# Kernel tuning notes

Hardware: AMD Instinct MI355X
Metric: run time of the kernel (lower is better)

## Reference

```python
import jax, jax.numpy as jnp
import numpy as np
from jax import lax

DISP = 4   # max displacement for correlation -> 81 channels
KSZ = 3    # deform/gate conv kernel size


def conv2d(x, w, b=None):
    out = lax.conv_general_dilated(x, w, (1, 1), 'SAME',
                                   dimension_numbers=('NCHW', 'OIHW', 'NCHW'))
    if b is not None:
        out = out + b[None, :, None, None]
    return out


def correlation(x1, x2, d=DISP):
    # FlowNet-style cost volume, kernel_size=1: per-displacement channel-mean dot product.
    B, C, H, W = x1.shape
    x2p = jnp.pad(x2, ((0, 0), (0, 0), (d, d), (d, d)))
    outs = []
    for dy in range(2 * d + 1):
        for dx in range(2 * d + 1):
            shifted = lax.dynamic_slice(x2p, (0, 0, dy, dx), (B, C, H, W))
            outs.append(jnp.sum(x1 * shifted, axis=1) / C)
    return jnp.stack(outs, axis=1)  # [B, (2d+1)^2, H, W]


def bilinear_sample(img, y, x):
    # img: [B,C,H,W]; y,x: [B,H,W] float sample coords; zero padding outside.
    B, C, H, W = img.shape
    y0 = jnp.floor(y); x0 = jnp.floor(x)
    y1 = y0 + 1.0;     x1 = x0 + 1.0
    wy1 = y - y0; wx1 = x - x0
    wy0 = 1.0 - wy1; wx0 = 1.0 - wx1
    flat = img.reshape(B, C, H * W)

    def gather(yi, xi):
        valid = (yi >= 0) & (yi <= H - 1) & (xi >= 0) & (xi <= W - 1)
        yc = jnp.clip(yi, 0, H - 1).astype(jnp.int32)
        xc = jnp.clip(xi, 0, W - 1).astype(jnp.int32)
        idx = (yc * W + xc).reshape(B, 1, H * W)
        g = jnp.take_along_axis(flat, idx, axis=2).reshape(B, C, H, W)
        return g * valid.astype(img.dtype)[:, None]

    return (gather(y0, x0) * (wy0 * wx0)[:, None]
          + gather(y0, x1) * (wy0 * wx1)[:, None]
          + gather(y1, x0) * (wy1 * wx0)[:, None]
          + gather(y1, x1) * (wy1 * wx1)[:, None])


def deform_conv(img, offset, w, k=KSZ):
    # offset: [B, 2*k*k, H, W] with (dy, dx) pairs per kernel tap (row-major).
    B, C, H, W = img.shape
    pad = (k - 1) // 2
    ys = jnp.arange(H, dtype=img.dtype)[None, :, None]
    xs = jnp.arange(W, dtype=img.dtype)[None, None, :]
    out = jnp.zeros((B, w.shape[0], H, W), dtype=img.dtype)
    for kk in range(k * k):
        ky, kx = kk // k, kk % k
        y = ys + (ky - pad) + offset[:, 2 * kk]
        x = xs + (kx - pad) + offset[:, 2 * kk + 1]
        s = bilinear_sample(img, y, x)
        out = out + jnp.einsum('oc,bchw->bohw', w[:, :, ky, kx], s)
    return out


def linear_scale(x, std_multiplier=3.0):
    pos = x > 0
    cnt = jnp.sum(pos).astype(x.dtype)
    mean = jnp.sum(jnp.where(pos, x, 0.0)) / jnp.maximum(cnt, 1.0)
    var = jnp.sum(jnp.where(pos, (x - mean) ** 2, 0.0)) / jnp.maximum(cnt - 1.0, 1.0)
    ub = mean + std_multiplier * jnp.sqrt(var)
    ub = jnp.where(cnt >= 2.0, ub, 1.0)  # matches torch nan / empty-positive fallback
    return jnp.clip(x, 0.0, lax.stop_gradient(ub)) / ub


def setup_inputs() -> dict:
    key = jax.random.key(0)
    ks = jax.random.split(key, 10)
    B, C, H, W = 8, 256, 64, 64
    f = jnp.float32
    inp = {
        'inputs':   jax.random.normal(ks[0], (B, C, H, W), f),
        'in_state': jax.random.normal(ks[1], (B, C, H, W), f),
        'w_reset':  jax.random.normal(ks[2], (C, 2 * C, 3, 3), f) * 0.02,
        'b_reset':  jnp.zeros((C,), f),
        'w_update': jax.random.normal(ks[3], (C, 2 * C, 3, 3), f) * 0.02,
        'b_update': jnp.zeros((C,), f),
        'w_out':    jax.random.normal(ks[4], (C, 2 * C, 3, 3), f) * 0.02,
        'b_out':    jnp.zeros((C,), f),
        'w_offset': jax.random.normal(ks[5], (18, 81, 1, 1), f) * 0.01,
        'w_align':  jax.random.normal(ks[6], (C, C, 3, 3), f) * 0.01,
    }
    return inp


def reference(inputs, in_state, w_reset, b_reset, w_update, b_update,
              w_out, b_out, w_offset, w_align):
    # align_features: correlation -> 1x1 offset conv -> deformable conv
    corr = correlation(inputs, in_state)
    offset = conv2d(corr, w_offset)
    aligned = deform_conv(in_state, offset, w_align)
    # ConvGRU gates with linear-scaled relu gates
    stacked = jnp.concatenate([inputs, aligned], axis=1)
    update = linear_scale(jax.nn.relu(conv2d(stacked, w_update, b_update)))
    reset = linear_scale(jax.nn.relu(conv2d(stacked, w_reset, b_reset)))
    out_in = jax.nn.relu(conv2d(jnp.concatenate([inputs, in_state * reset], axis=1), w_out, b_out))
    new_state = in_state * (1.0 - update) + out_in * update
    return (new_state, new_state)  # (out_feat, new_state)
```

## Files before the change

kernel.cpp:

```cpp
#include <hip/hip_runtime.h>
#include <stdint.h>
#include <math.h>

typedef unsigned short u16;
typedef short bf16x8 __attribute__((ext_vector_type(8)));
typedef float f32x4 __attribute__((ext_vector_type(4)));

#define MFMA16x16x32(a,b,c) __builtin_amdgcn_mfma_f32_16x16x32_bf16((a),(b),(c),0,0,0)

typedef __attribute__((address_space(3))) void as3_void;
typedef const __attribute__((address_space(1))) void as1_void;

__device__ __forceinline__ void g2l16(const void* g, void* l){
#if __has_builtin(__builtin_amdgcn_global_load_lds)
  __builtin_amdgcn_global_load_lds((as1_void*)g, (as3_void*)l, 16, 0, 0);
#else
  *(int4*)l = *(const int4*)g;
#endif
}

__device__ __forceinline__ u16 f2bf(float f){
  uint32_t u = __builtin_bit_cast(uint32_t, f);
  u += 0x7fffu + ((u >> 16) & 1u);
  return (u16)(u >> 16);
}
__device__ __forceinline__ float bf2f(u16 h){
  uint32_t u = ((uint32_t)h) << 16;
  return __builtin_bit_cast(float, u);
}
__device__ __forceinline__ void unpack8(int4 v, float* o){
  uint32_t w0=(uint32_t)v.x, w1=(uint32_t)v.y, w2=(uint32_t)v.z, w3=(uint32_t)v.w;
  o[0]=__builtin_bit_cast(float, w0<<16); o[1]=__builtin_bit_cast(float, w0&0xffff0000u);
  o[2]=__builtin_bit_cast(float, w1<<16); o[3]=__builtin_bit_cast(float, w1&0xffff0000u);
  o[4]=__builtin_bit_cast(float, w2<<16); o[5]=__builtin_bit_cast(float, w2&0xffff0000u);
  o[6]=__builtin_bit_cast(float, w3<<16); o[7]=__builtin_bit_cast(float, w3&0xffff0000u);
}
__device__ __forceinline__ int iclampi(int v,int lo,int hi){ return v<lo?lo:(v>hi?hi:v); }

__global__ void k_repack(const float* __restrict__ w_reset, const float* __restrict__ b_reset,
                         const float* __restrict__ w_update, const float* __restrict__ b_update,
                         const float* __restrict__ w_out, const float* __restrict__ w_offset,
                         const float* __restrict__ w_align,
                         u16* __restrict__ wgate, u16* __restrict__ wout,
                         u16* __restrict__ walign, float* __restrict__ woff,
                         float* __restrict__ biascat){
  int idx = blockIdx.x * 256 + threadIdx.x;
  if (idx < 512*4608){
    int e = idx & 7, j = (idx >> 3) & 2047, chunk = idx >> 14;
    int nb = chunk & 1, kk = chunk >> 1;
    int l = j & 15, q = (j >> 4) & 3, t16 = (j >> 6) & 15, ks2 = j >> 10;
    int n = nb*256 + t16*16 + l;
    int tap = kk >> 3, ksin = kk & 7;
    int c = ksin*64 + ks2*32 + q*8 + e;
    int ky = tap/3, kx = tap%3;
    float v = (n < 256) ? w_update[((n*512 + c)*3 + ky)*3 + kx]
                        : w_reset[(((n-256)*512 + c)*3 + ky)*3 + kx];
    wgate[idx] = f2bf(v);
  }
  if (idx < 256*4608){
    int e = idx & 7, j = (idx >> 3) & 1023, chunk = idx >> 13;
    int nb = chunk & 1, kk = chunk >> 1;
    int l = j & 15, q = (j >> 4) & 3, t8 = (j >> 6) & 7, ks2 = j >> 9;
    int n = nb*128 + t8*16 + l;
    int tap = kk >> 3, ksin = kk & 7;
    int c = ksin*64 + ks2*32 + q*8 + e;
    int ky = tap/3, kx = tap%3;
    wout[idx] = f2bf(w_out[((n*512 + c)*3 + ky)*3 + kx]);
  }
  if (idx < 256*2304){
    int u = idx >> 13, rem = idx & 8191;
    int n = rem >> 5, qd = (rem >> 3) & 3, e = idx & 7;
    int tap = u >> 3, ks = u & 7;
    int c = ks*32 + qd*8 + e;
    int ky = tap/3, kx = tap%3;
    walign[idx] = f2bf(w_align[((n*256 + c)*3 + ky)*3 + kx]);
  }
  if (idx < 1458) woff[idx] = w_offset[idx] * (1.f/256.f);
  if (idx < 512) biascat[idx] = (idx < 256) ? b_update[idx] : b_reset[idx-256];
}

__global__ __launch_bounds__(256) void k_transform(const float* __restrict__ inputs,
    const float* __restrict__ in_state, u16* __restrict__ stacked,
    u16* __restrict__ stacked2, u16* __restrict__ x2pad){
  __shared__ u16 t1[64*264];
  __shared__ u16 t2[64*264];
  int tid = threadIdx.x, bh = blockIdx.x;
  int b = bh >> 6, h = bh & 63;
  int w = tid & 63, cq = tid >> 6;
  for (int i = 0; i < 64; ++i){
    int c = i*4 + cq;
    int gi = ((b*256 + c)*64 + h)*64 + w;
    t1[w*264 + c] = f2bf(inputs[gi]);
    t2[w*264 + c] = f2bf(in_state[gi]);
  }
  __syncthreads();
  int px = tid >> 2, cg = tid & 3;
#pragma unroll
  for (int u = 0; u < 8; ++u){
    int c = cg*64 + u*8;
    int4 v1 = *(const int4*)(t1 + px*264 + c);
    int4 v2 = *(const int4*)(t2 + px*264 + c);
    *(int4*)(stacked  + (((b*66 + h+1)*66) + (px+1))*512 + c) = v1;
    *(int4*)(stacked2 + (((b*66 + h+1)*66) + (px+1))*512 + c) = v1;
    *(int4*)(x2pad    + (((b*72 + h+4)*72) + (px+4))*256 + c) = v2;
  }
}

__global__ __launch_bounds__(256) void k_corr(const u16* __restrict__ stacked,
    const u16* __restrict__ x2pad, float* __restrict__ corr){
  __shared__ u16 lA[8192];
  __shared__ u16 lB[32768];
  int tid = threadIdx.x, idx = blockIdx.x;
  int b = idx >> 6, ty = (idx >> 3) & 7, tx = idx & 7;
  int h0 = ty*8, w0 = tx*8;
  int wave = tid >> 6, lane = tid & 63, l15 = lane & 15, quad = lane >> 4;
  f32x4 acc[4][4];
#pragma unroll
  for (int i=0;i<4;i++)
#pragma unroll
    for (int j=0;j<4;j++){ f32x4 z = {0.f,0.f,0.f,0.f}; acc[i][j] = z; }

  for (int s = 0; s < 2; ++s){
#pragma unroll
    for (int i = 0; i < 4; ++i){
      int j = tid + i*256;
      int ml = j & 15, q = (j>>4)&3, mt = (j>>6)&3, ks = j >> 8;
      int px = mt*16 + ml, py = px >> 3, pxx = px & 7;
      const u16* g = stacked + (((b*66 + h0+py+1)*66) + (w0+pxx+1))*512 + s*128 + ks*32 + q*8;
      g2l16(g, lA + j*8);
    }
#pragma unroll
    for (int i = 0; i < 16; ++i){
      int j = tid + i*256;
      int nl = j & 15, q = (j>>4)&3, nt = (j>>6)&15, ks = j >> 10;
      int qp = nt*16 + nl, qy = qp >> 4, qx = qp & 15;
      const u16* g = x2pad + (((b*72 + h0+qy)*72) + (w0+qx))*256 + s*128 + ks*32 + q*8;
      g2l16(g, lB + j*8);
    }
    __syncthreads();
#pragma unroll
    for (int ks = 0; ks < 4; ++ks){
      bf16x8 bv[4];
#pragma unroll
      for (int ni=0; ni<4; ++ni){
        int nt = wave*4 + ni;
        bv[ni] = *(const bf16x8*)(lB + (((ks*16 + nt)*4 + quad)*16 + l15)*8);
      }
#pragma unroll
      for (int mi=0; mi<4; ++mi){
        bf16x8 av = *(const bf16x8*)(lA + (((ks*4 + mi)*4 + quad)*16 + l15)*8);
#pragma unroll
        for (int ni=0; ni<4; ++ni) acc[mi][ni] = MFMA16x16x32(av, bv[ni], acc[mi][ni]);
      }
    }
    __syncthreads();
  }
#pragma unroll
  for (int mi=0; mi<4; ++mi){
#pragma unroll
    for (int ni=0; ni<4; ++ni){
      int n = wave*64 + ni*16 + l15;
      int qy = n >> 4, qx = n & 15;
#pragma unroll
      for (int r=0; r<4; ++r){
        int m = mi*16 + quad*4 + r;
        int py = m >> 3, pxx = m & 7;
        int dy = qy - py, dx = qx - pxx;
        if ((unsigned)dy <= 8u && (unsigned)dx <= 8u)
          corr[(((b*64 + h0+py)*64) + (w0+pxx))*81 + dy*9 + dx] = acc[mi][ni][r];
      }
    }
  }
}

__global__ __launch_bounds__(256) void k_offset(const float* __restrict__ corr,
    const float* __restrict__ woff, float* __restrict__ offs){
  __shared__ float lc[32*84];
  __shared__ float lw[18*84];
  int tid = threadIdx.x, blk = blockIdx.x;
  int row = blk >> 1, half = blk & 1;
  int base = row*5184 + half*32*81;
  for (int i = tid; i < 32*81; i += 256){
    int px = i / 81, d = i % 81;
    lc[px*84 + d] = corr[base + i];
  }
  for (int i = tid; i < 18*84; i += 256){
    int o = i / 84, d = i % 84;
    if (d < 81) lw[i] = woff[o*81 + d];
  }
  __syncthreads();
  int px = tid & 31, og = tid >> 5;
  for (int o = og; o < 18; o += 8){
    float s = 0.f;
#pragma unroll
    for (int dd = 0; dd < 20; ++dd){
      float4 a = *(const float4*)(lc + px*84 + dd*4);
      float4 wv = *(const float4*)(lw + o*84 + dd*4);
      s += a.x*wv.x + a.y*wv.y + a.z*wv.z + a.w*wv.w;
    }
    s += lc[px*84 + 80] * lw[o*84 + 80];
    offs[(row*64 + half*32 + px)*18 + o] = s;
  }
}

__global__ __launch_bounds__(256) void k_deform(const u16* __restrict__ x2pad,
    const float* __restrict__ offs, const u16* __restrict__ walign,
    u16* __restrict__ stacked){
  __shared__ u16 lA[2][16384];
  int tid = threadIdx.x, bh = blockIdx.x;
  int b = bh >> 6, h = bh & 63;
  int wave = tid >> 6, lane = tid & 63, l15 = lane & 15, quad = lane >> 4;
  int g8 = tid >> 5, c32 = tid & 31;
  int ksw = c32 >> 2, qw = c32 & 3, x7 = c32 & 7;
  f32x4 acc[4][4];
#pragma unroll
  for (int i=0;i<4;i++)
#pragma unroll
    for (int j=0;j<4;j++){ f32x4 z = {0.f,0.f,0.f,0.f}; acc[i][j] = z; }

  auto STAGE = [&](u16* __restrict__ dst, int tap){
    int ky = tap/3, kx = tap - ky*3;
#pragma unroll 2
    for (int pi = 0; pi < 8; ++pi){
      int px = pi*8 + g8;
      float offy = offs[(bh*64 + px)*18 + 2*tap];
      float offx = offs[(bh*64 + px)*18 + 2*tap + 1];
      float y = (float)(h + ky - 1) + offy;
      float x = (float)(px + kx - 1) + offx;
      float y0f = floorf(y), x0f = floorf(x);
      float wy1 = y - y0f, wx1 = x - x0f;
      float wy0 = 1.f - wy1, wx0 = 1.f - wx1;
      int iy0 = iclampi((int)y0f, -4, 67), ix0 = iclampi((int)x0f, -4, 67);
      int iy1 = iclampi((int)y0f + 1, -4, 67), ix1 = iclampi((int)x0f + 1, -4, 67);
      const u16* p00 = x2pad + (((b*72 + iy0+4)*72) + (ix0+4))*256 + c32*8;
      const u16* p01 = x2pad + (((b*72 + iy0+4)*72) + (ix1+4))*256 + c32*8;
      const u16* p10 = x2pad + (((b*72 + iy1+4)*72) + (ix0+4))*256 + c32*8;
      const u16* p11 = x2pad + (((b*72 + iy1+4)*72) + (ix1+4))*256 + c32*8;
      int4 v00 = *(const int4*)p00;
      int4 v01 = *(const int4*)p01;
      int4 v10 = *(const int4*)p10;
      int4 v11 = *(const int4*)p11;
      float w00 = wy0*wx0, w01 = wy0*wx1, w10 = wy1*wx0, w11 = wy1*wx1;
      float a00[8], a01[8], a10[8], a11[8];
      unpack8(v00,a00); unpack8(v01,a01); unpack8(v10,a10); unpack8(v11,a11);
      union { u16 h2[8]; int4 v; } R;
#pragma unroll
      for (int jj = 0; jj < 8; ++jj)
        R.h2[jj] = f2bf(w00*a00[jj] + w01*a01[jj] + w10*a10[jj] + w11*a11[jj]);
      int mt = px >> 4, ml = px & 15;
      *(int4*)(dst + ksw*2048 + mt*512 + qw*128 + (ml ^ x7)*8) = R.v;
    }
  };

  STAGE(&lA[0][0], 0);
  __syncthreads();

  for (int tap = 0; tap < 9; ++tap){
    int d = tap & 1;
    if (tap < 8) STAGE(&lA[d^1][0], tap + 1);
    const u16* A = &lA[d][0];
    __builtin_amdgcn_s_setprio(1);
#pragma unroll
    for (int ks = 0; ks < 8; ++ks){
      bf16x8 bv[4];
#pragma unroll
      for (int ni=0; ni<4; ++ni){
        int n = wave*64 + ni*16 + l15;
        bv[ni] = *(const bf16x8*)(walign + (size_t)(tap*8 + ks)*8192 + n*32 + quad*8);
      }
#pragma unroll
      for (int mi=0; mi<4; ++mi){
        bf16x8 av = *(const bf16x8*)(A + ks*2048 + mi*512 + quad*128 + (l15 ^ ((ks*4 + quad) & 7))*8);
#pragma unroll
        for (int ni=0; ni<4; ++ni) acc[mi][ni] = MFMA16x16x32(av, bv[ni], acc[mi][ni]);
      }
    }
    __builtin_amdgcn_s_setprio(0);
    __syncthreads();
  }
#pragma unroll
  for (int mi=0; mi<4; ++mi){
#pragma unroll
    for (int ni=0; ni<4; ++ni){
      int n = wave*64 + ni*16 + l15;
#pragma unroll
      for (int r=0; r<4; ++r){
        int m = mi*16 + quad*4 + r;
        stacked[(((b*66 + h+1)*66) + (m+1))*512 + 256 + n] = f2bf(acc[mi][ni][r]);
      }
    }
  }
}

__device__ __forceinline__ void stageA_cl(u16* __restrict__ dst,
    const u16* __restrict__ in, int b, int h0, int kk, int tid){
  int tap = kk >> 3, ksin = kk & 7;
  int ky = tap/3, kx = tap - ky*3;
  const u16* abase = in + ((b*66 + h0 + ky)*66 + kx)*512 + ksin*64;
#pragma unroll
  for (int i = 0; i < 4; ++i){
    int j = i*512 + tid;
    int px = j >> 3, i8 = j & 7;
    int c8 = i8 ^ (px & 7);
    int r = px >> 6, w = px & 63;
    g2l16(abase + (r*66 + w)*512 + c8*8, dst + j*8);
  }
}
__device__ __forceinline__ void stageB16_k(u16* __restrict__ dst,
    const u16* __restrict__ wts, int nb, int kk, int ks2, int tid){
  const u16* wch = wts + (size_t)(kk*2 + nb) * 16384;
#pragma unroll
  for (int i = 0; i < 2; ++i){
    int j = (ks2<<10) | (i<<9) | tid;
    g2l16(wch + j*8, dst + j*8);
  }
}
__device__ __forceinline__ void stageB8_k(u16* __restrict__ dst,
    const u16* __restrict__ wts, int nb, int kk, int ks2, int tid){
  const u16* wch = wts + (size_t)(kk*2 + nb) * 8192;
  int j = (ks2<<9) | tid;
  g2l16(wch + j*8, dst + j*8);
}

#define AVREAD(RA, MROW, K2) \
  (*(const bf16x8*)((const u16*)(RA) + (MROW)*1024 + l15*64 + \
    ((((K2)*32) + quad*8) ^ ((l15 & 7)*8))))

#define PH16(CMH, AVC, BVC, AVN, BVN, LOADB, RA, RB, NMH, NK2, STG, EPI) do { \
  _Pragma("unroll") \
  for (int m4_=0;m4_<4;++m4_) \
    AVN[m4_] = AVREAD(RA, wm*8 + (NMH)*4 + m4_, NK2); \
  if (LOADB){ \
    _Pragma("unroll") \
    for (int ni_=0;ni_<4;++ni_) \
      BVN[ni_] = *(const bf16x8*)((const u16*)(RB) + ((((NK2)*16 + wn*4 + ni_)*4 + quad)*16 + l15)*8); \
  } \
  STG; \
  _Pragma("unroll") \
  for (int m4_=0;m4_<4;++m4_){ \
    _Pragma("unroll") \
    for (int ni_=0;ni_<4;++ni_) \
      acc[(CMH)*4+m4_][ni_] = MFMA16x16x32(AVC[m4_], BVC[ni_], acc[(CMH)*4+m4_][ni_]); \
  } \
  EPI; \
} while(0)

#define PH8Q(CMH, AVC, BVC, AVN, BVN, LOADB, RA, RB, NMH, NK2, STG, EPI) do { \
  _Pragma("unroll") \
  for (int m4_=0;m4_<4;++m4_) \
    AVN[m4_] = AVREAD(RA, wm*8 + (NMH)*4 + m4_, NK2); \
  if (LOADB){ \
    _Pragma("unroll") \
    for (int ni_=0;ni_<2;++ni_) \
      BVN[ni_] = *(const bf16x8*)((const u16*)(RB) + ((((NK2)*8 + wn*2 + ni_)*4 + quad)*16 + l15)*8); \
  } \
  STG; \
  _Pragma("unroll") \
  for (int m4_=0;m4_<4;++m4_){ \
    _Pragma("unroll") \
    for (int ni_=0;ni_<2;++ni_) \
      acc[(CMH)*4+m4_][ni_] = MFMA16x16x32(AVC[m4_], BVC[ni_], acc[(CMH)*4+m4_][ni_]); \
  } \
  EPI; \
} while(0)

#define SYNCTILE __syncthreads()

template<int NT, bool STATS>
__global__ __launch_bounds__(512, 2) void k_conv256(const u16* __restrict__ in,
    const u16* __restrict__ wts, const float* __restrict__ bias,
    u16* __restrict__ outp, float* __restrict__ partials){
  constexpr int NI = NT / 4;
  __shared__ u16 lA[2][16384];
  __shared__ u16 lB[2][NT*1024];

  int tid = threadIdx.x, g = blockIdx.x;
  int work = (g & 7) * 32 + (g >> 3);
  int nb = work >> 7, mt = work & 127;
  int b = mt >> 4, h0 = (mt & 15) * 4;
  int wave = tid >> 6, lane = tid & 63, l15 = lane & 15, quad = lane >> 4;
  int wm = wave & 1, wn = wave >> 1;

  f32x4 acc[8][NI];
#pragma unroll
  for (int i=0;i<8;i++)
#pragma unroll
    for (int j=0;j<NI;j++){ f32x4 z = {0.f,0.f,0.f,0.f}; acc[i][j] = z; }

  if constexpr (NT == 16){
    bf16x8 avA[4], avB[4], bvA[4], bvB[4];
    stageA_cl(&lA[0][0], in, b, h0, 0, tid);
    stageB16_k(&lB[0][0], wts, nb, 0, 0, tid);
    stageB16_k(&lB[0][0], wts, nb, 0, 1, tid);
    __syncthreads();
#pragma unroll
    for (int m4_=0;m4_<4;++m4_)
      avA[m4_] = AVREAD(&lA[0][0], wm*8 + m4_, 0);
#pragma unroll
    for (int ni_=0;ni_<4;++ni_)
      bvA[ni_] = *(const bf16x8*)(&lB[0][0] + (((wn*4 + ni_)*4 + quad)*16 + l15)*8);

#pragma unroll 1
    for (int t = 0; t < 72; ++t){
      int d = t & 1;
      const u16* Acur = &lA[d][0];
      const u16* Bcur = &lB[d][0];
      u16* Anx = &lA[d^1][0];
      u16* Bnx = &lB[d^1][0];
      bool hn = (t < 71);
      int kn = t + 1;
      PH16(0, avA, bvA, avB, bvB, 0, Acur, Bcur, 1, 0,
           if (hn){ stageA_cl(Anx, in, b, h0, kn, tid);
                    stageB16_k(Bnx, wts, nb, kn, 0, tid);
                    stageB16_k(Bnx, wts, nb, kn, 1, tid); }, );
      PH16(1, avB, bvA, avA, bvB, 1, Acur, Bcur, 0, 1, , );
      PH16(0, avA, bvB, avB, bvA, 0, Acur, Bcur, 1, 1, , SYNCTILE);
      PH16(1, avB, bvB, avA, bvA, 1, Anx, Bnx, 0, 0, , );
    }
  } else {
    bf16x8 avA[4], avB[4], bvA[2], bvB[2];
    stageA_cl(&lA[0][0], in, b, h0, 0, tid);
    stageB8_k(&lB[0][0], wts, nb, 0, 0, tid);
    stageB8_k(&lB[0][0], wts, nb, 0, 1, tid);
    __syncthreads();
#pragma unroll
    for (int m4_=0;m4_<4;++m4_)
      avA[m4_] = AVREAD(&lA[0][0], wm*8 + m4_, 0);
#pragma unroll
    for (int ni_=0;ni_<2;++ni_)
      bvA[ni_] = *(const bf16x8*)(&lB[0][0] + (((wn*2 + ni_)*4 + quad)*16 + l15)*8);

#pragma unroll 1
    for (int t = 0; t < 72; ++t){
      int d = t & 1;
      const u16* Acur = &lA[d][0];
      const u16* Bcur = &lB[d][0];
      u16* Anx = &lA[d^1][0];
      u16* Bnx = &lB[d^1][0];
      bool hn = (t < 71);
      int kn = t + 1;
      PH8Q(0, avA, bvA, avB, bvB, 0, Acur, Bcur, 1, 0,
           if (hn){ stageA_cl(Anx, in, b, h0, kn, tid);
                    stageB8_k(Bnx, wts, nb, kn, 0, tid);
                    stageB8_k(Bnx, wts, nb, kn, 1, tid); }, );
      PH8Q(1, avB, bvA, avA, bvB, 1, Acur, Bcur, 0, 1, , );
      PH8Q(0, avA, bvB, avB, bvA, 0, Acur, Bcur, 1, 1, , SYNCTILE);
      PH8Q(1, avB, bvB, avA, bvA, 1, Anx, Bnx, 0, 0, , );
    }
  }

  float bvl[NI];
#pragma unroll
  for (int ni = 0; ni < NI; ++ni)
    bvl[ni] = bias[nb*(NT*16) + wn*(NI*16) + ni*16 + l15];
  float sc = 0.f, ss = 0.f, sq = 0.f;
#pragma unroll
  for (int mi=0; mi<8; ++mi){
#pragma unroll
    for (int ni=0; ni<NI; ++ni){
      int n = nb*(NT*16) + wn*(NI*16) + ni*16 + l15;
#pragma unroll
      for (int r=0; r<4; ++r){
        int m = wm*128 + mi*16 + quad*4 + r;
        int row = h0 + (m >> 6), w = m & 63;
        float v = acc[mi][ni][r] + bvl[ni];
        v = fmaxf(v, 0.f);
        outp[(((b*64 + row)*64) + w)*(NT*32) + n] = f2bf(v);
        if (STATS){ sc += (v > 0.f) ? 1.f : 0.f; ss += v; sq += v*v; }
      }
    }
  }
  if constexpr (STATS){
    __shared__ float red[8][3];
#pragma unroll
    for (int off = 32; off; off >>= 1){
      sc += __shfl_down(sc, off); ss += __shfl_down(ss, off); sq += __shfl_down(sq, off);
    }
    if (lane == 0){ red[wave][0]=sc; red[wave][1]=ss; red[wave][2]=sq; }
    __syncthreads();
    if (tid == 0){
      float a0=0,a1=0,a2=0;
      for (int w2=0; w2<8; ++w2){ a0+=red[w2][0]; a1+=red[w2][1]; a2+=red[w2][2]; }
      partials[work*3+0]=a0; partials[work*3+1]=a1; partials[work*3+2]=a2;
    }
  }
}

__global__ __launch_bounds__(256) void k_finalize(const float* __restrict__ partials,
                                                  float* __restrict__ ubs){
  __shared__ float red[4][6];
  int tid = threadIdx.x, lane = tid & 63, wave = tid >> 6;
  float cu=0,su=0,qu=0,cr=0,sr=0,qr=0;
  {
    float c = partials[tid*3+0], s = partials[tid*3+1], q = partials[tid*3+2];
    if (tid < 128){ cu=c; su=s; qu=q; } else { cr=c; sr=s; qr=q; }
  }
#pragma unroll
  for (int off = 32; off; off >>= 1){
    cu += __shfl_down(cu, off); su += __shfl_down(su, off); qu += __shfl_down(qu, off);
    cr += __shfl_down(cr, off); sr += __shfl_down(sr, off); qr += __shfl_down(qr, off);
  }
  if (lane == 0){ red[wave][0]=cu; red[wave][1]=su; red[wave][2]=qu;
                  red[wave][3]=cr; red[wave][4]=sr; red[wave][5]=qr; }
  __syncthreads();
  if (tid < 2){
    double C=0, S=0, Q=0;
    for (int w2=0; w2<4; ++w2){
      C += red[w2][tid*3+0]; S += red[w2][tid*3+1]; Q += red[w2][tid*3+2];
    }
    float ub = 1.f;
    if (C >= 2.0){
      double mean = S / C;
      double var = (Q - C*mean*mean) / (C - 1.0);
      if (var < 0.0) var = 0.0;
      ub = (float)(mean + 3.0*sqrt(var));
    }
    ubs[tid] = ub;
    ubs[2+tid] = 1.f/ub;
  }
}

__global__ __launch_bounds__(256) void k_mulreset(const u16* __restrict__ G,
    const u16* __restrict__ x2pad, const float* __restrict__ ubs,
    u16* __restrict__ stacked2){
  int tid = threadIdx.x, bh = blockIdx.x;
  int b = bh >> 6, h = bh & 63;
  int px = tid >> 2, cg = tid & 3;
  float ubr = ubs[1], inv = ubs[3];
#pragma unroll
  for (int u = 0; u < 8; ++u){
    int c = cg*64 + u*8;
    int4 gv = *(const int4*)(G + (bh*64 + px)*512 + 256 + c);
    int4 sv = *(const int4*)(x2pad + (((b*72 + h+4)*72) + (px+4))*256 + c);
    float gf[8], sf[8]; unpack8(gv, gf); unpack8(sv, sf);
    union { u16 h2[8]; int4 v; } R;
#pragma unroll
    for (int j=0;j<8;j++){
      float r = fminf(gf[j], ubr) * inv;
      R.h2[j] = f2bf(sf[j] * r);
    }
    *(int4*)(stacked2 + (((b*66 + h+1)*66) + (px+1))*512 + 256 + c) = R.v;
  }
}

__global__ __launch_bounds__(256) void k_final(const u16* __restrict__ G,
    const u16* __restrict__ O, const float* __restrict__ in_state,
    const float* __restrict__ ubs, float* __restrict__ dout){
  __shared__ float Q[64*65];
  __shared__ float P[64*65];
  int tid = threadIdx.x, bh = blockIdx.x;
  int b = bh >> 6, h = bh & 63;
  float ubu = ubs[0], inv = ubs[2];
  int px = tid >> 2, cs = (tid & 3)*16;
  int w = tid & 63, c4 = tid >> 6;
  for (int cb = 0; cb < 4; ++cb){
#pragma unroll
    for (int tt = 0; tt < 2; ++tt){
      int cl = cs + tt*8;
      int c = cb*64 + cl;
      int4 gv = *(const int4*)(G + (bh*64 + px)*512 + c);
      int4 ov = *(const int4*)(O + (bh*64 + px)*256 + c);
      float gf[8], of[8]; unpack8(gv, gf); unpack8(ov, of);
#pragma unroll
      for (int j=0;j<8;j++){
        float u = fminf(gf[j], ubu) * inv;
        Q[px*65 + cl + j] = u;
        P[px*65 + cl + j] = of[j]*u;
      }
    }
    __syncthreads();
    for (int i = 0; i < 16; ++i){
      int cl = i*4 + c4;
      int c = cb*64 + cl;
      int gidx = (((b*256 + c)*64) + h)*64 + w;
      float s = in_state[gidx];
      float v = s*(1.f - Q[w*65 + cl]) + P[w*65 + cl];
      dout[gidx] = v;
      dout[8388608 + gidx] = v;
    }
    __syncthreads();
  }
}

extern "C" void kernel_launch(void* const* d_in, const int* in_sizes, int n_in,
                              void* d_out, int out_size, void* d_ws, size_t ws_size,
                              hipStream_t stream){
  (void)in_sizes; (void)n_in; (void)out_size; (void)ws_size;
  const float* inputs   = (const float*)d_in[0];
  const float* in_state = (const float*)d_in[1];
  const float* w_reset  = (const float*)d_in[2];
  const float* b_reset  = (const float*)d_in[3];
  const float* w_update = (const float*)d_in[4];
  const float* b_update = (const float*)d_in[5];
  const float* w_out    = (const float*)d_in[6];
  const float* b_out    = (const float*)d_in[7];
  const float* w_offset = (const float*)d_in[8];
  const float* w_align  = (const float*)d_in[9];
  float* dout = (float*)d_out;

  char* ws = (char*)d_ws;
  size_t off = 0;
  auto alloc = [&](size_t bytes)->char*{
    char* p = ws + off; off = (off + bytes + 255) & ~(size_t)255; return p;
  };
  const size_t x2pad_b   = 8ull*72*72*256*2;
  const size_t stacked_b = 8ull*66*66*512*2;
  u16* x2pad    = (u16*)alloc(x2pad_b);
  u16* stacked  = (u16*)alloc(stacked_b);
  u16* stacked2 = (u16*)alloc(stacked_b);
  float* corr   = (float*)alloc(8ull*64*64*81*4);
  float* offs   = (float*)alloc(8ull*64*64*18*4);
  u16* G        = (u16*)alloc(8ull*64*64*512*2);
  u16* O        = (u16*)alloc(8ull*64*64*256*2);
  u16* wgate    = (u16*)alloc(512ull*4608*2);
  u16* woutb    = (u16*)alloc(256ull*4608*2);
  u16* walignb  = (u16*)alloc(256ull*2304*2);
  float* woff   = (float*)alloc(1458*4);
  float* biascat= (float*)alloc(512*4);
  float* partials=(float*)alloc(1024*3*4);
  float* ubs    = (float*)alloc(4*4);

  hipMemsetAsync(x2pad,    0, x2pad_b,   stream);
  hipMemsetAsync(stacked,  0, stacked_b, stream);
  hipMemsetAsync(stacked2, 0, stacked_b, stream);

  k_repack<<<9216, 256, 0, stream>>>(w_reset, b_reset, w_update, b_update, w_out,
                                     w_offset, w_align, wgate, woutb, walignb, woff, biascat);
  k_transform<<<512, 256, 0, stream>>>(inputs, in_state, stacked, stacked2, x2pad);
  k_corr<<<512, 256, 0, stream>>>(stacked, x2pad, corr);
  k_offset<<<1024, 256, 0, stream>>>(corr, woff, offs);
  k_deform<<<512, 256, 0, stream>>>(x2pad, offs, walignb, stacked);
  k_conv256<16, true><<<256, 512, 0, stream>>>(stacked, wgate, biascat, G, partials);
  k_finalize<<<1, 256, 0, stream>>>(partials, ubs);
  k_mulreset<<<512, 256, 0, stream>>>(G, x2pad, ubs, stacked2);
  k_conv256<8, false><<<256, 512, 0, stream>>>(stacked2, woutb, b_out, O, nullptr);
  k_final<<<512, 256, 0, stream>>>(G, O, in_state, ubs, dout);
}
```

Before: 583.4 us.

## Halve conv M-tile, read weights directly from global, double grid size

The implicit-GEMM conv kernel now tiles 128 output pixels (2 rows) instead of 256, which doubles the grid to 512 blocks. It drops LDS staging of the weight tiles and loads B fragments straight from global memory (relying on cache), which shrinks shared memory so launch bounds can ask for 4 blocks per CU. The finalize kernel is adjusted to the new partials layout. The aim is more parallelism and occupancy, at the cost of less weight reuse per block and more global and cache traffic for B operands.

```diff
diff --git a/kernel.cpp b/kernel.cpp
--- a/kernel.cpp
+++ b/kernel.cpp
@@ -292,13 +292,13 @@
   }
 }
 
-__device__ __forceinline__ void stageA_cl(u16* __restrict__ dst,
+__device__ __forceinline__ void stageA128(u16* __restrict__ dst,
     const u16* __restrict__ in, int b, int h0, int kk, int tid){
   int tap = kk >> 3, ksin = kk & 7;
   int ky = tap/3, kx = tap - ky*3;
   const u16* abase = in + ((b*66 + h0 + ky)*66 + kx)*512 + ksin*64;
 #pragma unroll
-  for (int i = 0; i < 4; ++i){
+  for (int i = 0; i < 2; ++i){
     int j = i*512 + tid;
     int px = j >> 3, i8 = j & 7;
     int c8 = i8 ^ (px & 7);
@@ -306,147 +306,89 @@
     g2l16(abase + (r*66 + w)*512 + c8*8, dst + j*8);
   }
 }
-__device__ __forceinline__ void stageB16_k(u16* __restrict__ dst,
-    const u16* __restrict__ wts, int nb, int kk, int ks2, int tid){
-  const u16* wch = wts + (size_t)(kk*2 + nb) * 16384;
-#pragma unroll
-  for (int i = 0; i < 2; ++i){
-    int j = (ks2<<10) | (i<<9) | tid;
-    g2l16(wch + j*8, dst + j*8);
-  }
-}
-__device__ __forceinline__ void stageB8_k(u16* __restrict__ dst,
-    const u16* __restrict__ wts, int nb, int kk, int ks2, int tid){
-  const u16* wch = wts + (size_t)(kk*2 + nb) * 8192;
-  int j = (ks2<<9) | tid;
-  g2l16(wch + j*8, dst + j*8);
-}
 
 #define AVREAD(RA, MROW, K2) \
   (*(const bf16x8*)((const u16*)(RA) + (MROW)*1024 + l15*64 + \
     ((((K2)*32) + quad*8) ^ ((l15 & 7)*8))))
 
-#define PH16(CMH, AVC, BVC, AVN, BVN, LOADB, RA, RB, NMH, NK2, STG, EPI) do { \
-  _Pragma("unroll") \
-  for (int m4_=0;m4_<4;++m4_) \
-    AVN[m4_] = AVREAD(RA, wm*8 + (NMH)*4 + m4_, NK2); \
-  if (LOADB){ \
-    _Pragma("unroll") \
-    for (int ni_=0;ni_<4;++ni_) \
-      BVN[ni_] = *(const bf16x8*)((const u16*)(RB) + ((((NK2)*16 + wn*4 + ni_)*4 + quad)*16 + l15)*8); \
-  } \
-  STG; \
-  _Pragma("unroll") \
-  for (int m4_=0;m4_<4;++m4_){ \
-    _Pragma("unroll") \
-    for (int ni_=0;ni_<4;++ni_) \
-      acc[(CMH)*4+m4_][ni_] = MFMA16x16x32(AVC[m4_], BVC[ni_], acc[(CMH)*4+m4_][ni_]); \
-  } \
-  EPI; \
-} while(0)
-
-#define PH8Q(CMH, AVC, BVC, AVN, BVN, LOADB, RA, RB, NMH, NK2, STG, EPI) do { \
-  _Pragma("unroll") \
-  for (int m4_=0;m4_<4;++m4_) \
-    AVN[m4_] = AVREAD(RA, wm*8 + (NMH)*4 + m4_, NK2); \
-  if (LOADB){ \
-    _Pragma("unroll") \
-    for (int ni_=0;ni_<2;++ni_) \
-      BVN[ni_] = *(const bf16x8*)((const u16*)(RB) + ((((NK2)*8 + wn*2 + ni_)*4 + quad)*16 + l15)*8); \
-  } \
-  STG; \
-  _Pragma("unroll") \
-  for (int m4_=0;m4_<4;++m4_){ \
-    _Pragma("unroll") \
-    for (int ni_=0;ni_<2;++ni_) \
-      acc[(CMH)*4+m4_][ni_] = MFMA16x16x32(AVC[m4_], BVC[ni_], acc[(CMH)*4+m4_][ni_]); \
-  } \
-  EPI; \
-} while(0)
-
-#define SYNCTILE __syncthreads()
+#define BVG(WCH, NI_, K2) \
+  (*(const bf16x8*)((WCH) + ((((K2)*NT + wn*NI + (NI_))*64) + quad*16 + l15)*8))
 
 template<int NT, bool STATS>
-__global__ __launch_bounds__(512, 2) void k_conv256(const u16* __restrict__ in,
+__global__ __launch_bounds__(512, 4) void k_conv256(const u16* __restrict__ in,
     const u16* __restrict__ wts, const float* __restrict__ bias,
     u16* __restrict__ outp, float* __restrict__ partials){
   constexpr int NI = NT / 4;
-  __shared__ u16 lA[2][16384];
-  __shared__ u16 lB[2][NT*1024];
+  __shared__ u16 lA[2][8192];
 
   int tid = threadIdx.x, g = blockIdx.x;
-  int work = (g & 7) * 32 + (g >> 3);
-  int nb = work >> 7, mt = work & 127;
-  int b = mt >> 4, h0 = (mt & 15) * 4;
+  int work = (g & 7) * 64 + (g >> 3);
+  int nb = work >> 8, mt = work & 255;
+  int b = mt >> 5, h0 = (mt & 31) * 2;
   int wave = tid >> 6, lane = tid & 63, l15 = lane & 15, quad = lane >> 4;
   int wm = wave & 1, wn = wave >> 1;
 
-  f32x4 acc[8][NI];
-#pragma unroll
-  for (int i=0;i<8;i++)
+  f32x4 acc[4][NI];
+#pragma unroll
+  for (int i=0;i<4;i++)
 #pragma unroll
     for (int j=0;j<NI;j++){ f32x4 z = {0.f,0.f,0.f,0.f}; acc[i][j] = z; }
 
-  if constexpr (NT == 16){
-    bf16x8 avA[4], avB[4], bvA[4], bvB[4];
-    stageA_cl(&lA[0][0], in, b, h0, 0, tid);
-    stageB16_k(&lB[0][0], wts, nb, 0, 0, tid);
-    stageB16_k(&lB[0][0], wts, nb, 0, 1, tid);
-    __syncthreads();
-#pragma unroll
-    for (int m4_=0;m4_<4;++m4_)
-      avA[m4_] = AVREAD(&lA[0][0], wm*8 + m4_, 0);
-#pragma unroll
-    for (int ni_=0;ni_<4;++ni_)
-      bvA[ni_] = *(const bf16x8*)(&lB[0][0] + (((wn*4 + ni_)*4 + quad)*16 + l15)*8);
+  bf16x8 avA[2], avB[2], bvA[NI], bvB[NI];
+
+  stageA128(&lA[0][0], in, b, h0, 0, tid);
+  __syncthreads();
+  {
+    const u16* wch0 = wts + (size_t)nb * (NT*1024);
+#pragma unroll
+    for (int m2=0;m2<2;++m2) avA[m2] = AVREAD(&lA[0][0], wm*4 + m2, 0);
+#pragma unroll
+    for (int ni=0;ni<NI;++ni) bvA[ni] = BVG(wch0, ni, 0);
+  }
 
 #pragma unroll 1
-    for (int t = 0; t < 72; ++t){
-      int d = t & 1;
-      const u16* Acur = &lA[d][0];
-      const u16* Bcur = &lB[d][0];
-      u16* Anx = &lA[d^1][0];
-      u16* Bnx = &lB[d^1][0];
-      bool hn = (t < 71);
-      int kn = t + 1;
-      PH16(0, avA, bvA, avB, bvB, 0, Acur, Bcur, 1, 0,
-           if (hn){ stageA_cl(Anx, in, b, h0, kn, tid);
-                    stageB16_k(Bnx, wts, nb, kn, 0, tid);
-                    stageB16_k(Bnx, wts, nb, kn, 1, tid); }, );
-      PH16(1, avB, bvA, avA, bvB, 1, Acur, Bcur, 0, 1, , );
-      PH16(0, avA, bvB, avB, bvA, 0, Acur, Bcur, 1, 1, , SYNCTILE);
-      PH16(1, avB, bvB, avA, bvA, 1, Anx, Bnx, 0, 0, , );
-    }
-  } else {
-    bf16x8 avA[4], avB[4], bvA[2], bvB[2];
-    stageA_cl(&lA[0][0], in, b, h0, 0, tid);
-    stageB8_k(&lB[0][0], wts, nb, 0, 0, tid);
-    stageB8_k(&lB[0][0], wts, nb, 0, 1, tid);
-    __syncthreads();
-#pragma unroll
-    for (int m4_=0;m4_<4;++m4_)
-      avA[m4_] = AVREAD(&lA[0][0], wm*8 + m4_, 0);
-#pragma unroll
-    for (int ni_=0;ni_<2;++ni_)
-      bvA[ni_] = *(const bf16x8*)(&lB[0][0] + (((wn*2 + ni_)*4 + quad)*16 + l15)*8);
-
-#pragma unroll 1
-    for (int t = 0; t < 72; ++t){
-      int d = t & 1;
-      const u16* Acur = &lA[d][0];
-      const u16* Bcur = &lB[d][0];
-      u16* Anx = &lA[d^1][0];
-      u16* Bnx = &lB[d^1][0];
-      bool hn = (t < 71);
-      int kn = t + 1;
-      PH8Q(0, avA, bvA, avB, bvB, 0, Acur, Bcur, 1, 0,
-           if (hn){ stageA_cl(Anx, in, b, h0, kn, tid);
-                    stageB8_k(Bnx, wts, nb, kn, 0, tid);
-                    stageB8_k(Bnx, wts, nb, kn, 1, tid); }, );
-      PH8Q(1, avB, bvA, avA, bvB, 1, Acur, Bcur, 0, 1, , );
-      PH8Q(0, avA, bvB, avB, bvA, 0, Acur, Bcur, 1, 1, , SYNCTILE);
-      PH8Q(1, avB, bvB, avA, bvA, 1, Anx, Bnx, 0, 0, , );
-    }
+  for (int t = 0; t < 72; ++t){
+    int d = t & 1;
+    const u16* Acur = &lA[d][0];
+    u16* Anx = &lA[d^1][0];
+    bool hn = (t < 71);
+    int kn = hn ? (t + 1) : t;
+    const u16* wchC = wts + (size_t)(t*2 + nb) * (NT*1024);
+    const u16* wchN = wts + (size_t)(kn*2 + nb) * (NT*1024);
+#pragma unroll
+    for (int m2=0;m2<2;++m2) avB[m2] = AVREAD(Acur, wm*4 + 2 + m2, 0);
+    if (hn) stageA128(Anx, in, b, h0, kn, tid);
+#pragma unroll
+    for (int m2=0;m2<2;++m2)
+#pragma unroll
+      for (int ni=0;ni<NI;++ni)
+        acc[m2][ni] = MFMA16x16x32(avA[m2], bvA[ni], acc[m2][ni]);
+#pragma unroll
+    for (int m2=0;m2<2;++m2) avA[m2] = AVREAD(Acur, wm*4 + m2, 1);
+#pragma unroll
+    for (int ni=0;ni<NI;++ni) bvB[ni] = BVG(wchC, ni, 1);
+#pragma unroll
+    for (int m2=0;m2<2;++m2)
+#pragma unroll
+      for (int ni=0;ni<NI;++ni)
+        acc[2+m2][ni] = MFMA16x16x32(avB[m2], bvA[ni], acc[2+m2][ni]);
+#pragma unroll
+    for (int m2=0;m2<2;++m2) avB[m2] = AVREAD(Acur, wm*4 + 2 + m2, 1);
+#pragma unroll
+    for (int m2=0;m2<2;++m2)
+#pragma unroll
+      for (int ni=0;ni<NI;++ni)
+        acc[m2][ni] = MFMA16x16x32(avA[m2], bvB[ni], acc[m2][ni]);
+    __syncthreads();
+#pragma unroll
+    for (int m2=0;m2<2;++m2) avA[m2] = AVREAD(Anx, wm*4 + m2, 0);
+#pragma unroll
+    for (int ni=0;ni<NI;++ni) bvA[ni] = BVG(wchN, ni, 0);
+#pragma unroll
+    for (int m2=0;m2<2;++m2)
+#pragma unroll
+      for (int ni=0;ni<NI;++ni)
+        acc[2+m2][ni] = MFMA16x16x32(avB[m2], bvB[ni], acc[2+m2][ni]);
   }
 
   float bvl[NI];
@@ -455,13 +397,13 @@
     bvl[ni] = bias[nb*(NT*16) + wn*(NI*16) + ni*16 + l15];
   float sc = 0.f, ss = 0.f, sq = 0.f;
 #pragma unroll
-  for (int mi=0; mi<8; ++mi){
+  for (int mi=0; mi<4; ++mi){
 #pragma unroll
     for (int ni=0; ni<NI; ++ni){
       int n = nb*(NT*16) + wn*(NI*16) + ni*16 + l15;
 #pragma unroll
       for (int r=0; r<4; ++r){
-        int m = wm*128 + mi*16 + quad*4 + r;
+        int m = wm*64 + mi*16 + quad*4 + r;
         int row = h0 + (m >> 6), w = m & 63;
         float v = acc[mi][ni][r] + bvl[ni];
         v = fmaxf(v, 0.f);
@@ -490,11 +432,8 @@
                                                   float* __restrict__ ubs){
   __shared__ float red[4][6];
   int tid = threadIdx.x, lane = tid & 63, wave = tid >> 6;
-  float cu=0,su=0,qu=0,cr=0,sr=0,qr=0;
-  {
-    float c = partials[tid*3+0], s = partials[tid*3+1], q = partials[tid*3+2];
-    if (tid < 128){ cu=c; su=s; qu=q; } else { cr=c; sr=s; qr=q; }
-  }
+  float cu = partials[tid*3+0], su = partials[tid*3+1], qu = partials[tid*3+2];
+  float cr = partials[(256+tid)*3+0], sr = partials[(256+tid)*3+1], qr = partials[(256+tid)*3+2];
 #pragma unroll
   for (int off = 32; off; off >>= 1){
     cu += __shfl_down(cu, off); su += __shfl_down(su, off); qu += __shfl_down(qu, off);
@@ -630,9 +569,9 @@
   k_corr<<<512, 256, 0, stream>>>(stacked, x2pad, corr);
   k_offset<<<1024, 256, 0, stream>>>(corr, woff, offs);
   k_deform<<<512, 256, 0, stream>>>(x2pad, offs, walignb, stacked);
-  k_conv256<16, true><<<256, 512, 0, stream>>>(stacked, wgate, biascat, G, partials);
+  k_conv256<16, true><<<512, 512, 0, stream>>>(stacked, wgate, biascat, G, partials);
   k_finalize<<<1, 256, 0, stream>>>(partials, ubs);
   k_mulreset<<<512, 256, 0, stream>>>(G, x2pad, ubs, stacked2);
-  k_conv256<8, false><<<256, 512, 0, stream>>>(stacked2, woutb, b_out, O, nullptr);
+  k_conv256<8, false><<<512, 512, 0, stream>>>(stacked2, woutb, b_out, O, nullptr);
   k_final<<<512, 256, 0, stream>>>(G, O, in_state, ubs, dout);
 }
```

Result: no change. 587.5 us (+0.7%).
